# Kernel tuning notes

Hardware: AMD Instinct MI355X
Metric: run time of the kernel (lower is better)

## Reference

```python
import jax, jax.numpy as jnp
import numpy as np

B, L, D = 64, 128, 768          # batch, padded seq len, bert dim
H, HA = 1024, 256               # d_label_hidden, d_label_hidden_arc
POS, V = 18, 40                 # pos vocab, arc (deprel) vocab


def setup_inputs() -> dict:
    key = jax.random.key(0)
    ks = jax.random.split(key, 24)
    n = lambda i, shape, s=0.02: jax.random.normal(ks[i], shape, jnp.float32) * s
    # realistic padding: random sentence lengths in [L//2, L]
    lengths = jax.random.randint(ks[1], (B,), L // 2, L + 1)
    pad_mask = (jnp.arange(L)[None, :] < lengths[:, None]).astype(jnp.float32)
    heads = jax.random.randint(ks[2], (B, L), 0, L)
    # mark padded positions as -1 (zero head vector), as in the original loop
    heads = jnp.where(pad_mask > 0, heads, -1)
    return {
        "ann": jax.random.normal(ks[0], (B, L, D), jnp.float32),
        "pad_mask": pad_mask,
        "correct_heads": heads,
        # label-biaffine branch (hidden H)
        "W_head_mlp": n(3, (D, H)), "b_head_mlp": n(4, (H,)),
        "W_dep_mlp": n(5, (D, H)), "b_dep_mlp": n(6, (H,)),
        "W_lin": n(7, (H, H)), "b_lin": n(8, (H,)),
        "head_vec": n(9, (H,), 1.0), "dep_vec": n(10, (H,), 1.0),
        "bias": n(11, (1, 1, 1), 1.0),
        # arc-label biaffine branch (hidden HA, per-label bilinear)
        "W_head_arc_mlp": n(12, (D, HA)), "b_head_arc_mlp": n(13, (HA,)),
        "W_dep_arc_mlp": n(14, (D, HA)), "b_dep_arc_mlp": n(15, (HA,)),
        "W_arc": n(16, (V, HA, HA), 1.0),
        "head_vec_arc": n(17, (HA, V), 1.0), "dep_vec_arc": n(18, (HA, V), 1.0),
        "bias_arc": n(19, (1, 1, V), 1.0),
        # POS tip
        "W_pos": n(20, (D, POS)), "b_pos": n(21, (POS,)),
    }


def reference(ann, pad_mask, correct_heads,
              W_head_mlp, b_head_mlp, W_dep_mlp, b_dep_mlp,
              W_lin, b_lin, head_vec, dep_vec, bias,
              W_head_arc_mlp, b_head_arc_mlp, W_dep_arc_mlp, b_dep_arc_mlp,
              W_arc, head_vec_arc, dep_vec_arc, bias_arc,
              W_pos, b_pos):
    # POS prediction
    pos_pred = ann @ W_pos + b_pos                                  # [B,L,POS]

    # ---- dependency (unlabeled arc) biaffine ----
    ann_head = jax.nn.relu(ann @ W_head_mlp + b_head_mlp)           # [B,L,H]
    ann_dep = jax.nn.relu(ann @ W_dep_mlp + b_dep_mlp)              # [B,L,H]
    head_bias = ann_head @ head_vec                                 # [B,L]
    dep_bias = ann_dep @ dep_vec                                    # [B,L]
    Wh = ann_head @ W_lin + b_lin                                   # [B,L,H]
    # scores[b,i,j] = dep[b,i] . Wh[b,j]
    dep_W_headT = jnp.einsum('bih,bjh->bij', ann_dep, Wh)
    dep_W_headT = dep_W_headT + head_bias[:, None, :] + dep_bias[:, :, None] + bias
    valid_head = pad_mask[:, None, :] > 0                           # [B,1,L]
    dep_W_headT = jnp.where(valid_head, dep_W_headT, -jnp.inf)

    # ---- labeled arc biaffine (gather gold head per dependent) ----
    ann_head_arc = jax.nn.relu(ann @ W_head_arc_mlp + b_head_arc_mlp)  # [B,L,HA]
    ann_dep_arc = jax.nn.relu(ann @ W_dep_arc_mlp + b_dep_arc_mlp)     # [B,L,HA]
    idx = jnp.clip(correct_heads, 0, L - 1)
    gathered = jnp.take_along_axis(ann_head_arc, idx[:, :, None], axis=1)
    gathered = jnp.where((correct_heads == -1)[:, :, None], 0.0, gathered)  # [B,L,HA]

    head_arc_bias = gathered @ head_vec_arc                         # [B,L,V]
    dep_arc_bias = ann_dep_arc @ dep_vec_arc                        # [B,L,V]
    # per-label bilinear: s[b,l,v] = gathered[b,l] . W_arc[v] . dep[b,l]
    dep_W_headT_arc = jnp.einsum('bld,vde,ble->blv', gathered, W_arc, ann_dep_arc)
    dep_W_headT_arc = dep_W_headT_arc + head_arc_bias + dep_arc_bias + bias_arc

    return pos_pred, dep_W_headT, dep_W_headT_arc
```

## Files before the change

### kernel.cpp

```cpp
#include <hip/hip_runtime.h>
#include <hip/hip_bf16.h>

#define B_ 64
#define L_ 128
#define D_ 768
#define H_ 1024
#define HA_ 256
#define POS_ 18
#define V_ 40
#define BL_ (B_ * L_)

#define NEG_BIG (-1.0e30f)

typedef __attribute__((ext_vector_type(8))) short short8v;
typedef __attribute__((ext_vector_type(4))) short short4v;
typedef __attribute__((ext_vector_type(4))) float f32x4;

__device__ inline void split_bf16(float x, short& hi, short& lo) {
  __hip_bfloat16 h = __float2bfloat16(x);
  hi = *reinterpret_cast<short*>(&h);
  const float r = x - __bfloat162float(h);
  __hip_bfloat16 l = __float2bfloat16(r);
  lo = *reinterpret_cast<short*>(&l);
}

__device__ __forceinline__ short f2b(float x) {
  __hip_bfloat16 h = __float2bfloat16(x);
  return *reinterpret_cast<short*>(&h);
}
__device__ __forceinline__ float b2f(short s) {
  __hip_bfloat16 h = *reinterpret_cast<__hip_bfloat16*>(&s);
  return __bfloat162float(h);
}

__device__ __forceinline__ int swz8(int row, int s) { return ((s + (row >> 1)) & 3) * 8; }
__device__ __forceinline__ int colswz(int row, int n) {
  return (n & ~31) + swz8(row, (n >> 3) & 3) + (n & 7);
}

__device__ __forceinline__ void ld_lds16(const void* g, void* l) {
  __builtin_amdgcn_global_load_lds(
      (const __attribute__((address_space(1))) unsigned int*)g,
      (__attribute__((address_space(3))) unsigned int*)l, 16, 0, 0);
}

template<bool RELU, bool HASBIAS>
__global__ __launch_bounds__(256)
void gemm_bias(const float* __restrict__ A, const float* __restrict__ Bm,
               const float* __restrict__ bias, float* __restrict__ C,
               int M, int N, int K) {
  __shared__ __align__(16) float As[16][68];
  __shared__ __align__(16) float Bs[16][68];
  const int t = threadIdx.x;
  const int tx = t & 15, ty = t >> 4;
  const int m0 = blockIdx.y * 64, n0 = blockIdx.x * 64;
  const int arow = t >> 2, aks = (t & 3) * 4;
  const int bkr = t >> 4, bns = (t & 15) * 4;
  float acc[4][4] = {};
  for (int k0 = 0; k0 < K; k0 += 16) {
    const float4 av = *reinterpret_cast<const float4*>(&A[(size_t)(m0 + arow) * K + k0 + aks]);
    float4 bv;
    const int nb = n0 + bns;
    if (nb + 3 < N) {
      bv = *reinterpret_cast<const float4*>(&Bm[(size_t)(k0 + bkr) * N + nb]);
    } else {
      bv.x = (nb + 0 < N) ? Bm[(size_t)(k0 + bkr) * N + nb + 0] : 0.f;
      bv.y = (nb + 1 < N) ? Bm[(size_t)(k0 + bkr) * N + nb + 1] : 0.f;
      bv.z = (nb + 2 < N) ? Bm[(size_t)(k0 + bkr) * N + nb + 2] : 0.f;
      bv.w = 0.f;
    }
    __syncthreads();
    As[aks + 0][arow] = av.x;
    As[aks + 1][arow] = av.y;
    As[aks + 2][arow] = av.z;
    As[aks + 3][arow] = av.w;
    *reinterpret_cast<float4*>(&Bs[bkr][bns]) = bv;
    __syncthreads();
#pragma unroll
    for (int kk = 0; kk < 16; ++kk) {
      const float4 a4 = *reinterpret_cast<const float4*>(&As[kk][ty * 4]);
      const float4 b4 = *reinterpret_cast<const float4*>(&Bs[kk][tx * 4]);
      const float aa[4] = {a4.x, a4.y, a4.z, a4.w};
      const float bb[4] = {b4.x, b4.y, b4.z, b4.w};
#pragma unroll
      for (int i = 0; i < 4; ++i)
#pragma unroll
        for (int j = 0; j < 4; ++j)
          acc[i][j] = fmaf(aa[i], bb[j], acc[i][j]);
    }
  }
#pragma unroll
  for (int j = 0; j < 4; ++j) {
    const int n = n0 + tx * 4 + j;
    if (n >= N) continue;
    float bj = 0.f;
    if constexpr (HASBIAS) bj = bias[n];
#pragma unroll
    for (int i = 0; i < 4; ++i) {
      const int m = m0 + ty * 4 + i;
      float v = acc[i][j] + bj;
      if (RELU) v = fmaxf(v, 0.f);
      C[(size_t)m * N + n] = v;
    }
  }
}

__global__ __launch_bounds__(256)
void split_pre(const float* __restrict__ src, short* __restrict__ hi,
               short* __restrict__ lo, int K) {
  const int t = threadIdx.x;
  const int r = blockIdx.x * 4 + (t >> 6);
  const int lane = t & 63;
  for (int c = lane * 4; c < K; c += 256) {
    const float4 v = *reinterpret_cast<const float4*>(&src[(size_t)r * K + c]);
    const float vv[4] = {v.x, v.y, v.z, v.w};
    short4v h4, l4;
#pragma unroll
    for (int j = 0; j < 4; ++j) {
      short h, l;
      split_bf16(vv[j], h, l);
      h4[j] = h; l4[j] = l;
    }
    const int cs = colswz(r, c);
    *reinterpret_cast<short4v*>(&hi[(size_t)r * K + cs]) = h4;
    *reinterpret_cast<short4v*>(&lo[(size_t)r * K + cs]) = l4;
  }
}

__global__ __launch_bounds__(256)
void megaprep(const float* __restrict__ Whm, const float* __restrict__ Wdm,
              const float* __restrict__ Wlin, const float* __restrict__ Wha,
              const float* __restrict__ Wda, const float* __restrict__ Wpos,
              short* __restrict__ Thm, short* __restrict__ Tdm,
              short* __restrict__ Tlin, short* __restrict__ Tha,
              short* __restrict__ Tda, short* __restrict__ Pth,
              short* __restrict__ Ptl) {
  __shared__ float tile[32][33];
  const int bid = blockIdx.x;
  const int t = threadIdx.x;
  if (bid < 2944) {
    const float* W; short* T; int K, N, local;
    if (bid < 768)       { W = Whm;  T = Thm;  K = D_; N = H_;  local = bid; }
    else if (bid < 1536) { W = Wdm;  T = Tdm;  K = D_; N = H_;  local = bid - 768; }
    else if (bid < 2560) { W = Wlin; T = Tlin; K = H_; N = H_;  local = bid - 1536; }
    else if (bid < 2752) { W = Wha;  T = Tha;  K = D_; N = HA_; local = bid - 2560; }
    else                 { W = Wda;  T = Tda;  K = D_; N = HA_; local = bid - 2752; }
    const int ntiles = N >> 5;
    const int n0 = (local % ntiles) * 32;
    const int k0 = (local / ntiles) * 32;
    const int r = t >> 3, c = (t & 7) * 4;
    const float4 w4 = *reinterpret_cast<const float4*>(&W[(size_t)(k0 + r) * N + n0 + c]);
    tile[r][c + 0] = w4.x;
    tile[r][c + 1] = w4.y;
    tile[r][c + 2] = w4.z;
    tile[r][c + 3] = w4.w;
    __syncthreads();
    short4v hi4;
#pragma unroll
    for (int j = 0; j < 4; ++j) hi4[j] = f2b(tile[c + j][r]);
    const int row = n0 + r;
    const int cs = swz8(row, (c >> 3) & 3) + (c & 7);
    *reinterpret_cast<short4v*>(&T[(size_t)row * K + k0 + cs]) = hi4;
  } else {
    const int k0 = (bid - 2944) * 32;
    const int n = t & 31;
    const int ks = (t >> 5) * 4;
#pragma unroll
    for (int j = 0; j < 4; ++j) {
      const int k = k0 + ks + j;
      const float v = (n < POS_) ? Wpos[(size_t)k * POS_ + n] : 0.f;
      short h, l;
      split_bf16(v, h, l);
      Pth[(size_t)n * D_ + colswz(n, k)] = h;
      Ptl[(size_t)n * D_ + colswz(n, k)] = l;
    }
  }
}

__global__ __launch_bounds__(256)
void gemm_h2x(const short* __restrict__ Ath, const short* __restrict__ Atl,
              const short* __restrict__ B1h, const short* __restrict__ B2h,
              const float* __restrict__ bias1h, const float* __restrict__ bias2h,
              short* __restrict__ O1h, short* __restrict__ O2h,
              const short* __restrict__ B1a, const short* __restrict__ B2a,
              const float* __restrict__ bias1a, const float* __restrict__ bias2a,
              float* __restrict__ O1a, float* __restrict__ O2a,
              const short* __restrict__ Pth, const short* __restrict__ Ptl,
              const float* __restrict__ bpos, float* __restrict__ outp) {
  __shared__ __align__(16) short AhP[2][2048];
  __shared__ __align__(16) short B1P[2][4096];
  __shared__ __align__(16) short B2P[2][4096];
  const int bid = blockIdx.x;
  const int t = threadIdx.x;
  const int lane = t & 63, w = t >> 6;
  const int fr = lane & 15, kgi = lane >> 4;
  const int drow = lane >> 2, dslot = lane & 3;

  if (bid < 1280) {
    const bool big = bid < 1024;
    const int N = big ? H_ : HA_;
    const int ntx = N >> 7;
    const int local = big ? bid : bid - 1024;
    const int m0 = (local / ntx) * 64, n0 = (local % ntx) * 128;
    const short* B1t = big ? B1h : B1a;
    const short* B2t = big ? B2h : B2a;
    const float* bias1v = big ? bias1h : bias1a;
    const float* bias2v = big ? bias2h : bias2a;
    const int wm = w >> 1, wn = w & 1;
    f32x4 acc1[2][4] = {};
    f32x4 acc2[2][4] = {};

    auto stage = [&](int tt, int pb) {
      const int k0 = tt << 5;
      {
        const size_t ga = (size_t)(m0 + w * 16 + drow) * D_ + k0 + dslot * 8;
        ld_lds16(&Ath[ga], &AhP[pb][w * 512]);
      }
#pragma unroll
      for (int cc = 0; cc < 2; ++cc) {
        const int c = w * 2 + cc;
        const size_t gb = (size_t)(n0 + c * 16 + drow) * D_ + k0 + dslot * 8;
        ld_lds16(&B1t[gb], &B1P[pb][c * 512]);
        ld_lds16(&B2t[gb], &B2P[pb][c * 512]);
      }
    };
    auto compute = [&](int pb) {
      short8v ah[2];
#pragma unroll
      for (int mi = 0; mi < 2; ++mi) {
        const int r = wm * 32 + mi * 16 + fr;
        ah[mi] = *reinterpret_cast<const short8v*>(&AhP[pb][r * 32 + swz8(r, kgi)]);
      }
      __builtin_amdgcn_s_setprio(1);
#pragma unroll
      for (int nj = 0; nj < 4; ++nj) {
        const int rn = wn * 64 + nj * 16 + fr;
        const int sw = swz8(rn, kgi);
        const short8v b1 = *reinterpret_cast<const short8v*>(&B1P[pb][rn * 32 + sw]);
        const short8v b2 = *reinterpret_cast<const short8v*>(&B2P[pb][rn * 32 + sw]);
#pragma unroll
        for (int mi = 0; mi < 2; ++mi) {
          acc1[mi][nj] = __builtin_amdgcn_mfma_f32_16x16x32_bf16(ah[mi], b1, acc1[mi][nj], 0, 0, 0);
          acc2[mi][nj] = __builtin_amdgcn_mfma_f32_16x16x32_bf16(ah[mi], b2, acc2[mi][nj], 0, 0, 0);
        }
      }
      __builtin_amdgcn_s_setprio(0);
    };

    stage(0, 0);
    int cur = 0;
    for (int tt = 0; tt < 24; ++tt) {
      if (tt + 1 < 24) {
        stage(tt + 1, cur ^ 1);
        asm volatile("s_waitcnt vmcnt(5)" ::: "memory");
      } else {
        asm volatile("s_waitcnt vmcnt(0)" ::: "memory");
      }
      __builtin_amdgcn_s_barrier();
      compute(cur);
      __builtin_amdgcn_s_barrier();
      cur ^= 1;
    }

    const int rg = lane >> 4;
#pragma unroll
    for (int nj = 0; nj < 4; ++nj) {
      const int n = n0 + wn * 64 + nj * 16 + fr;
      const float b1 = bias1v[n];
      const float b2 = bias2v[n];
#pragma unroll
      for (int mi = 0; mi < 2; ++mi) {
#pragma unroll
        for (int q = 0; q < 4; ++q) {
          const int m = m0 + wm * 32 + mi * 16 + rg * 4 + q;
          const float v1 = fmaxf(acc1[mi][nj][q] + b1, 0.f);
          const float v2 = fmaxf(acc2[mi][nj][q] + b2, 0.f);
          if (big) {
            const size_t o = (size_t)m * N + colswz(m, n);
            O1h[o] = f2b(v1);
            O2h[o] = f2b(v2);
          } else {
            O1a[(size_t)m * N + n] = v1;
            O2a[(size_t)m * N + n] = v2;
          }
        }
      }
    }
  } else {
    const int m0 = (bid - 1280) * 64;
    f32x4 acc[2] = {};

    auto stage = [&](int tt, int pb) {
      const int k0 = tt << 5;
      const size_t ga = (size_t)(m0 + w * 16 + drow) * D_ + k0 + dslot * 8;
      ld_lds16(&Ath[ga], &AhP[pb][w * 512]);
      ld_lds16(&Atl[ga], &B1P[pb][w * 512]);
      {
        const short* bsrc = (w & 2) ? Ptl : Pth;
        const int c = w & 1;
        const size_t gb = (size_t)(c * 16 + drow) * D_ + k0 + dslot * 8;
        ld_lds16(&bsrc[gb], &B2P[pb][(w & 2) * 512 + c * 512]);
      }
    };
    auto compute = [&](int pb) {
      const int r = w * 16 + fr;
      const int swa = swz8(r, kgi);
      const short8v ah = *reinterpret_cast<const short8v*>(&AhP[pb][r * 32 + swa]);
      const short8v al = *reinterpret_cast<const short8v*>(&B1P[pb][r * 32 + swa]);
#pragma unroll
      for (int nj = 0; nj < 2; ++nj) {
        const int rn = nj * 16 + fr;
        const int sw = swz8(rn, kgi);
        const short8v bh = *reinterpret_cast<const short8v*>(&B2P[pb][rn * 32 + sw]);
        const short8v bl = *reinterpret_cast<const short8v*>(&B2P[pb][1024 + rn * 32 + sw]);
        acc[nj] = __builtin_amdgcn_mfma_f32_16x16x32_bf16(ah, bh, acc[nj], 0, 0, 0);
        acc[nj] = __builtin_amdgcn_mfma_f32_16x16x32_bf16(al, bh, acc[nj], 0, 0, 0);
        acc[nj] = __builtin_amdgcn_mfma_f32_16x16x32_bf16(ah, bl, acc[nj], 0, 0, 0);
      }
    };

    stage(0, 0);
    int cur = 0;
    for (int tt = 0; tt < 24; ++tt) {
      if (tt + 1 < 24) {
        stage(tt + 1, cur ^ 1);
        asm volatile("s_waitcnt vmcnt(3)" ::: "memory");
      } else {
        asm volatile("s_waitcnt vmcnt(0)" ::: "memory");
      }
      __builtin_amdgcn_s_barrier();
      compute(cur);
      __builtin_amdgcn_s_barrier();
      cur ^= 1;
    }

    const int rg = lane >> 4;
#pragma unroll
    for (int nj = 0; nj < 2; ++nj) {
      const int n = nj * 16 + fr;
      if (n >= POS_) continue;
      const float bj = bpos[n];
#pragma unroll
      for (int q = 0; q < 4; ++q) {
        const int m = m0 + w * 16 + rg * 4 + q;
        outp[(size_t)m * POS_ + n] = acc[nj][q] + bj;
      }
    }
  }
}

__global__ __launch_bounds__(256)
void lin_bias(const short* __restrict__ Ahh, const short* __restrict__ Bth,
              const float* __restrict__ bias, short* __restrict__ Oh,
              const short* __restrict__ Adh,
              const float* __restrict__ head_vec, const float* __restrict__ dep_vec,
              float* __restrict__ hb, float* __restrict__ db) {
  __shared__ __align__(16) short AhP[2][2048];
  __shared__ __align__(16) short BhP[2][4096];
  const int bid = blockIdx.x;
  const int t = threadIdx.x;
  const int lane = t & 63, w = t >> 6;

  if (bid < 1024) {
    const int m0 = (bid >> 3) * 64, n0 = (bid & 7) * 128;
    const int wm = w >> 1, wn = w & 1;
    const int fr = lane & 15, kgi = lane >> 4;
    const int drow = lane >> 2, dslot = lane & 3;
    f32x4 acc[2][4] = {};

    auto stage = [&](int tt, int pb) {
      const int k0 = tt << 5;
      {
        const size_t ga = (size_t)(m0 + w * 16 + drow) * H_ + k0 + dslot * 8;
        ld_lds16(&Ahh[ga], &AhP[pb][w * 512]);
      }
#pragma unroll
      for (int cc = 0; cc < 2; ++cc) {
        const int c = w * 2 + cc;
        const size_t gb = (size_t)(n0 + c * 16 + drow) * H_ + k0 + dslot * 8;
        ld_lds16(&Bth[gb], &BhP[pb][c * 512]);
      }
    };
    auto compute = [&](int pb) {
      short8v ah[2];
#pragma unroll
      for (int mi = 0; mi < 2; ++mi) {
        const int r = wm * 32 + mi * 16 + fr;
        ah[mi] = *reinterpret_cast<const short8v*>(&AhP[pb][r * 32 + swz8(r, kgi)]);
      }
      __builtin_amdgcn_s_setprio(1);
#pragma unroll
      for (int nj = 0; nj < 4; ++nj) {
        const int rn = wn * 64 + nj * 16 + fr;
        const short8v bh = *reinterpret_cast<const short8v*>(&BhP[pb][rn * 32 + swz8(rn, kgi)]);
#pragma unroll
        for (int mi = 0; mi < 2; ++mi)
          acc[mi][nj] = __builtin_amdgcn_mfma_f32_16x16x32_bf16(ah[mi], bh, acc[mi][nj], 0, 0, 0);
      }
      __builtin_amdgcn_s_setprio(0);
    };

    stage(0, 0);
    int cur = 0;
    for (int tt = 0; tt < 32; ++tt) {
      if (tt + 1 < 32) {
        stage(tt + 1, cur ^ 1);
        asm volatile("s_waitcnt vmcnt(3)" ::: "memory");
      } else {
        asm volatile("s_waitcnt vmcnt(0)" ::: "memory");
      }
      __builtin_amdgcn_s_barrier();
      compute(cur);
      __builtin_amdgcn_s_barrier();
      cur ^= 1;
    }

    const int rg = lane >> 4;
#pragma unroll
    for (int nj = 0; nj < 4; ++nj) {
      const int n = n0 + wn * 64 + nj * 16 + fr;
      const float bj = bias[n];
#pragma unroll
      for (int mi = 0; mi < 2; ++mi) {
#pragma unroll
        for (int q = 0; q < 4; ++q) {
          const int m = m0 + wm * 32 + mi * 16 + rg * 4 + q;
          Oh[(size_t)m * H_ + colswz(m, n)] = f2b(acc[mi][nj][q] + bj);
        }
      }
    }
  } else {
    const int m = (bid - 1024) * 4 + w;
    float sh = 0.f, sd = 0.f;
#pragma unroll
    for (int jj = 0; jj < 4; ++jj) {
      const int c = lane * 16 + jj * 4;
      const size_t o = (size_t)m * H_ + colswz(m, c);
      const short4v h4 = *reinterpret_cast<const short4v*>(&Ahh[o]);
      const short4v d4 = *reinterpret_cast<const short4v*>(&Adh[o]);
      const float4 hv = *reinterpret_cast<const float4*>(&head_vec[c]);
      const float4 dv = *reinterpret_cast<const float4*>(&dep_vec[c]);
      const float hvv[4] = {hv.x, hv.y, hv.z, hv.w};
      const float dvv[4] = {dv.x, dv.y, dv.z, dv.w};
#pragma unroll
      for (int j = 0; j < 4; ++j) {
        sh = fmaf(b2f(h4[j]), hvv[j], sh);
        sd = fmaf(b2f(d4[j]), dvv[j], sd);
      }
    }
#pragma unroll
    for (int off = 32; off; off >>= 1) {
      sh += __shfl_xor(sh, off);
      sd += __shfl_xor(sd, off);
    }
    if (lane == 0) {
      hb[m] = sh;
      db[m] = sd;
    }
  }
}

__global__ __launch_bounds__(256)
void scores_h(const short* __restrict__ Adh, const short* __restrict__ Whh,
              const float* __restrict__ hb, const float* __restrict__ db,
              const float* __restrict__ pad_mask, const float* __restrict__ bias1,
              float* __restrict__ out2) {
  __shared__ __align__(16) short AhP[2][2048];
  __shared__ __align__(16) short BhP[2][2048];
  const int t = threadIdx.x;
  const int b = blockIdx.z;
  const int i0 = blockIdx.y * 64, j0 = blockIdx.x * 64;
  const int lane = t & 63, w = t >> 6;
  const int wm = w >> 1, wn = w & 1;
  const int fr = lane & 15, kgi = lane >> 4;
  const int drow = lane >> 2, dslot = lane & 3;
  const size_t abase = ((size_t)b * L_ + i0) * H_;
  const size_t bbase = ((size_t)b * L_ + j0) * H_;
  f32x4 acc[2][2] = {};

  auto stage = [&](int tt, int pb) {
    const int k0 = tt << 5;
    const size_t ga = abase + (size_t)(w * 16 + drow) * H_ + k0 + dslot * 8;
    ld_lds16(&Adh[ga], &AhP[pb][w * 512]);
    const size_t gb = bbase + (size_t)(w * 16 + drow) * H_ + k0 + dslot * 8;
    ld_lds16(&Whh[gb], &BhP[pb][w * 512]);
  };
  auto compute = [&](int pb) {
    short8v ah[2];
#pragma unroll
    for (int mi = 0; mi < 2; ++mi) {
      const int r = wm * 32 + mi * 16 + fr;
      ah[mi] = *reinterpret_cast<const short8v*>(&AhP[pb][r * 32 + swz8(r, kgi)]);
    }
    __builtin_amdgcn_s_setprio(1);
#pragma unroll
    for (int nj = 0; nj < 2; ++nj) {
      const int rn = wn * 32 + nj * 16 + fr;
      const short8v bh = *reinterpret_cast<const short8v*>(&BhP[pb][rn * 32 + swz8(rn, kgi)]);
#pragma unroll
      for (int mi = 0; mi < 2; ++mi)
        acc[mi][nj] = __builtin_amdgcn_mfma_f32_16x16x32_bf16(ah[mi], bh, acc[mi][nj], 0, 0, 0);
    }
    __builtin_amdgcn_s_setprio(0);
  };

  stage(0, 0);
  int cur = 0;
  for (int tt = 0; tt < 32; ++tt) {
    if (tt + 1 < 32) {
      stage(tt + 1, cur ^ 1);
      asm volatile("s_waitcnt vmcnt(2)" ::: "memory");
    } else {
      asm volatile("s_waitcnt vmcnt(0)" ::: "memory");
    }
    __builtin_amdgcn_s_barrier();
    compute(cur);
    __builtin_amdgcn_s_barrier();
    cur ^= 1;
  }

  const int rg = lane >> 4;
  const float bias0 = bias1[0];
#pragma unroll
  for (int nj = 0; nj < 2; ++nj) {
    const int jcol = j0 + wn * 32 + nj * 16 + fr;
    const float mj = pad_mask[b * L_ + jcol];
    const float hbj = hb[b * L_ + jcol];
#pragma unroll
    for (int mi = 0; mi < 2; ++mi) {
#pragma unroll
      for (int q = 0; q < 4; ++q) {
        const int irow = i0 + wm * 32 + mi * 16 + rg * 4 + q;
        float v = acc[mi][nj][q] + hbj + db[b * L_ + irow] + bias0;
        if (!(mj > 0.f)) v = NEG_BIG;
        out2[((size_t)b * L_ + irow) * L_ + jcol] = v;
      }
    }
  }
}

__global__ __launch_bounds__(256)
void arcprep(const float* __restrict__ Warc, const float* __restrict__ dv,
             const float* __restrict__ head_arcb, const int* __restrict__ heads,
             short* __restrict__ WtA, float* __restrict__ dvT,
             float* __restrict__ g32, short* __restrict__ g_hi) {
  __shared__ float tile[32][33];
  const int bid = blockIdx.x;
  const int t = threadIdx.x;
  if (bid < 2560) {
    const int v = bid >> 6, rem = bid & 63;
    const int d0 = (rem >> 3) * 32, e0 = (rem & 7) * 32;
    const int r = t >> 3, c = (t & 7) * 4;
    const float4 w4 = *reinterpret_cast<const float4*>(
        &Warc[((size_t)v * HA_ + d0 + r) * HA_ + e0 + c]);
    tile[r][c + 0] = w4.x;
    tile[r][c + 1] = w4.y;
    tile[r][c + 2] = w4.z;
    tile[r][c + 3] = w4.w;
    __syncthreads();
    short4v hi4;
#pragma unroll
    for (int j = 0; j < 4; ++j) hi4[j] = f2b(tile[c + j][r]);
    const int row = e0 + r;
    const int cs = swz8(row, (c >> 3) & 3) + (c & 7);
    *reinterpret_cast<short4v*>(&WtA[((size_t)v * HA_ + row) * HA_ + d0 + cs]) = hi4;
  } else if (bid < 2600) {
    const int v = bid - 2560;
    dvT[(size_t)v * HA_ + t] = dv[(size_t)t * V_ + v];
  } else {
    const int m = (bid - 2600) * 4 + (t >> 6);
    const int lane = t & 63;
    const int h = heads[m];
    float4 g4 = make_float4(0.f, 0.f, 0.f, 0.f);
    if (h >= 0)
      g4 = *reinterpret_cast<const float4*>(
          &head_arcb[((size_t)((m >> 7) * L_ + h)) * HA_ + lane * 4]);
    *reinterpret_cast<float4*>(&g32[(size_t)m * HA_ + lane * 4]) = g4;
    short4v hi4;
    const float gv[4] = {g4.x, g4.y, g4.z, g4.w};
#pragma unroll
    for (int j = 0; j < 4; ++j) hi4[j] = f2b(gv[j]);
    *reinterpret_cast<short4v*>(&g_hi[(size_t)m * HA_ + colswz(m, lane * 4)]) = hi4;
  }
}

__global__ __launch_bounds__(512)
void arc_h(const short* __restrict__ g_hi, const short* __restrict__ Wt_hi,
           const float* __restrict__ dep32, const float* __restrict__ hb_arc,
           const float* __restrict__ dvT, float* __restrict__ out3) {
  __shared__ __align__(16) short AhP[2][8192];
  __shared__ __align__(16) short BhP[2][8192];
  __shared__ float parts[256][2];
  const int t = threadIdx.x;
  const int bid = blockIdx.x;
  const int xcd = bid & 7;
  const int j = bid >> 3;
  const int m0 = (j / 5) * 256;
  const int v = xcd * 5 + (j % 5);
  const int lane = t & 63, w = t >> 6;
  const int wm = w >> 1, we = w & 1;
  const int fr = lane & 15, kgi = lane >> 4;
  const int drow = lane >> 2, dslot = lane & 3;
  const size_t wbase = (size_t)v * HA_ * HA_;

  f32x4 acc[4][8] = {};

  auto stage = [&](int tt, int pb) {
    const int k0 = tt << 5;
#pragma unroll
    for (int cc = 0; cc < 2; ++cc) {
      const int c = w * 2 + cc;
      const size_t ga = (size_t)(m0 + c * 16 + drow) * HA_ + k0 + dslot * 8;
      ld_lds16(&g_hi[ga], &AhP[pb][c * 512]);
      const size_t gb = wbase + (size_t)(c * 16 + drow) * HA_ + k0 + dslot * 8;
      ld_lds16(&Wt_hi[gb], &BhP[pb][c * 512]);
    }
  };
  auto compute = [&](int pb) {
    short8v ah[4];
#pragma unroll
    for (int mi = 0; mi < 4; ++mi) {
      const int r = wm * 64 + mi * 16 + fr;
      ah[mi] = *reinterpret_cast<const short8v*>(&AhP[pb][r * 32 + swz8(r, kgi)]);
    }
    __builtin_amdgcn_s_setprio(1);
#pragma unroll
    for (int ej = 0; ej < 8; ++ej) {
      const int rb = we * 128 + ej * 16 + fr;
      const short8v bh = *reinterpret_cast<const short8v*>(&BhP[pb][rb * 32 + swz8(rb, kgi)]);
#pragma unroll
      for (int mi = 0; mi < 4; ++mi)
        acc[mi][ej] = __builtin_amdgcn_mfma_f32_16x16x32_bf16(ah[mi], bh, acc[mi][ej], 0, 0, 0);
    }
    __builtin_amdgcn_s_setprio(0);
  };

  stage(0, 0);
  int cur = 0;
#pragma unroll
  for (int tt = 0; tt < 8; ++tt) {
    if (tt < 7) {
      stage(tt + 1, cur ^ 1);
      asm volatile("s_waitcnt vmcnt(4)" ::: "memory");
    } else {
      asm volatile("s_waitcnt vmcnt(0)" ::: "memory");
    }
    __builtin_amdgcn_s_barrier();
    compute(cur);
    __builtin_amdgcn_s_barrier();
    cur ^= 1;
  }

  const int rg = lane >> 4;
  float dvr[8];
#pragma unroll
  for (int ej = 0; ej < 8; ++ej)
    dvr[ej] = dvT[(size_t)v * HA_ + we * 128 + ej * 16 + fr];
#pragma unroll
  for (int mi = 0; mi < 4; ++mi) {
#pragma unroll
    for (int q = 0; q < 4; ++q) {
      const int mrow = wm * 64 + mi * 16 + rg * 4 + q;
      const int m = m0 + mrow;
      float s = 0.f;
#pragma unroll
      for (int ej = 0; ej < 8; ++ej)
        s = fmaf(acc[mi][ej][q] + dvr[ej],
                 dep32[(size_t)m * HA_ + we * 128 + ej * 16 + fr], s);
      s += __shfl_xor(s, 1, 16);
      s += __shfl_xor(s, 2, 16);
      s += __shfl_xor(s, 4, 16);
      s += __shfl_xor(s, 8, 16);
      if (fr == 0) parts[mrow][we] = s;
    }
  }
  __syncthreads();
  if (t < 256) {
    const int m = m0 + t;
    out3[(size_t)m * V_ + v] = parts[t][0] + parts[t][1] + hb_arc[(size_t)m * V_ + v];
  }
}

extern "C" void kernel_launch(void* const* d_in, const int* in_sizes, int n_in,
                              void* d_out, int out_size, void* d_ws, size_t ws_size,
                              hipStream_t stream) {
  const float* ann        = (const float*)d_in[0];
  const float* pad_mask   = (const float*)d_in[1];
  const int*   heads      = (const int*)d_in[2];
  const float* W_head_mlp = (const float*)d_in[3];
  const float* b_head_mlp = (const float*)d_in[4];
  const float* W_dep_mlp  = (const float*)d_in[5];
  const float* b_dep_mlp  = (const float*)d_in[6];
  const float* W_lin      = (const float*)d_in[7];
  const float* b_lin      = (const float*)d_in[8];
  const float* head_vec   = (const float*)d_in[9];
  const float* dep_vec    = (const float*)d_in[10];
  const float* bias1      = (const float*)d_in[11];
  const float* W_head_arc = (const float*)d_in[12];
  const float* b_head_arc = (const float*)d_in[13];
  const float* W_dep_arc  = (const float*)d_in[14];
  const float* b_dep_arc  = (const float*)d_in[15];
  const float* W_arc      = (const float*)d_in[16];
  const float* hv_arc     = (const float*)d_in[17];
  const float* dv_arc     = (const float*)d_in[18];
  const float* bias_arc   = (const float*)d_in[19];
  const float* W_pos      = (const float*)d_in[20];
  const float* b_pos      = (const float*)d_in[21];

  float* out_pos    = (float*)d_out;
  float* out_scores = out_pos + (size_t)BL_ * POS_;
  float* out_arc    = out_scores + (size_t)B_ * L_ * L_;

  float* ws  = (float*)d_ws;
  float* R1  = ws;
  float* R2  = R1 + (size_t)BL_ * H_;
  float* R3  = R2 + (size_t)BL_ * H_;
  float* head_arcb = R3 + (size_t)BL_ * H_;
  float* dep_arcb  = head_arcb + (size_t)BL_ * HA_;
  float* hb        = dep_arcb + (size_t)BL_ * HA_;
  float* db        = hb + BL_;
  short* wt0     = (short*)(db + BL_);
  short* Wth_hm  = wt0;
  short* Wth_dm  = Wth_hm + (size_t)H_ * D_;
  short* Wth_lin = Wth_dm + (size_t)H_ * D_;
  short* Wth_ha  = Wth_lin + (size_t)H_ * H_;
  short* Wth_da  = Wth_ha + (size_t)HA_ * D_;
  short* Pth     = Wth_da + (size_t)HA_ * D_;
  short* Ptl     = Pth + (size_t)32 * D_;
  short* Ahh = (short*)R1;
  short* Adh = (short*)R2;
  short* Ath = (short*)R3;  short* Atl = Ath + (size_t)BL_ * D_;
  short* Whh = (short*)R3;
  float* g32 = (float*)wt0;
  short* Wt_hi  = (short*)R1;
  short* g_hi   = Wt_hi + (size_t)V_ * HA_ * HA_;
  float* hb_arc = (float*)(g_hi + (size_t)BL_ * HA_);
  float* dvT    = hb_arc + (size_t)BL_ * V_;

  const dim3 blk(256);
  split_pre<<<dim3(BL_ / 4), blk, 0, stream>>>(ann, Ath, Atl, D_);
  megaprep<<<dim3(2968), blk, 0, stream>>>(
      W_head_mlp, W_dep_mlp, W_lin, W_head_arc, W_dep_arc, W_pos,
      Wth_hm, Wth_dm, Wth_lin, Wth_ha, Wth_da, Pth, Ptl);

  gemm_h2x<<<dim3(1408), blk, 0, stream>>>(
      Ath, Atl, Wth_hm, Wth_dm, b_head_mlp, b_dep_mlp, Ahh, Adh,
      Wth_ha, Wth_da, b_head_arc, b_dep_arc, head_arcb, dep_arcb,
      Pth, Ptl, b_pos, out_pos);

  lin_bias<<<dim3(3072), blk, 0, stream>>>(
      Ahh, Wth_lin, b_lin, Whh, Adh, head_vec, dep_vec, hb, db);

  scores_h<<<dim3(2, 2, B_), blk, 0, stream>>>(
      Adh, Whh, hb, db, pad_mask, bias1, out_scores);

  arcprep<<<dim3(4648), blk, 0, stream>>>(
      W_arc, dv_arc, head_arcb, heads, Wt_hi, dvT, g32, g_hi);
  gemm_bias<false, true><<<dim3(1, BL_ / 64), blk, 0, stream>>>(
      g32, hv_arc, bias_arc, hb_arc, BL_, V_, HA_);
  arc_h<<<dim3((BL_ / 256) * V_), dim3(512), 0, stream>>>(
      g_hi, Wt_hi, dep_arcb, hb_arc, dvT, out_arc);
}
```

Baseline: 243.8 us.

## Merge arc-prep and scores kernels, compute head-arc bias before gather

The head-arc bias GEMM now runs on the ungathered head_arcb inside extra blocks of lin_bias, and arc_h gathers that bias through the gold head index. The gather fp32 copy g32 is no longer written. scores_h and arcprep are folded into a single scoresarc launch with block-index dispatch, which removes two launches and lets the small arc-prep work share the GPU with the scores GEMM. The cost is larger heterogeneous kernels and an extra indexed load in the arc_h epilogue.

```diff
diff --git a/kernel.cpp b/kernel.cpp
--- a/kernel.cpp
+++ b/kernel.cpp
@@ -42,67 +42,6 @@
   __builtin_amdgcn_global_load_lds(
       (const __attribute__((address_space(1))) unsigned int*)g,
       (__attribute__((address_space(3))) unsigned int*)l, 16, 0, 0);
-}
-
-template<bool RELU, bool HASBIAS>
-__global__ __launch_bounds__(256)
-void gemm_bias(const float* __restrict__ A, const float* __restrict__ Bm,
-               const float* __restrict__ bias, float* __restrict__ C,
-               int M, int N, int K) {
-  __shared__ __align__(16) float As[16][68];
-  __shared__ __align__(16) float Bs[16][68];
-  const int t = threadIdx.x;
-  const int tx = t & 15, ty = t >> 4;
-  const int m0 = blockIdx.y * 64, n0 = blockIdx.x * 64;
-  const int arow = t >> 2, aks = (t & 3) * 4;
-  const int bkr = t >> 4, bns = (t & 15) * 4;
-  float acc[4][4] = {};
-  for (int k0 = 0; k0 < K; k0 += 16) {
-    const float4 av = *reinterpret_cast<const float4*>(&A[(size_t)(m0 + arow) * K + k0 + aks]);
-    float4 bv;
-    const int nb = n0 + bns;
-    if (nb + 3 < N) {
-      bv = *reinterpret_cast<const float4*>(&Bm[(size_t)(k0 + bkr) * N + nb]);
-    } else {
-      bv.x = (nb + 0 < N) ? Bm[(size_t)(k0 + bkr) * N + nb + 0] : 0.f;
-      bv.y = (nb + 1 < N) ? Bm[(size_t)(k0 + bkr) * N + nb + 1] : 0.f;
-      bv.z = (nb + 2 < N) ? Bm[(size_t)(k0 + bkr) * N + nb + 2] : 0.f;
-      bv.w = 0.f;
-    }
-    __syncthreads();
-    As[aks + 0][arow] = av.x;
-    As[aks + 1][arow] = av.y;
-    As[aks + 2][arow] = av.z;
-    As[aks + 3][arow] = av.w;
-    *reinterpret_cast<float4*>(&Bs[bkr][bns]) = bv;
-    __syncthreads();
-#pragma unroll
-    for (int kk = 0; kk < 16; ++kk) {
-      const float4 a4 = *reinterpret_cast<const float4*>(&As[kk][ty * 4]);
-      const float4 b4 = *reinterpret_cast<const float4*>(&Bs[kk][tx * 4]);
-      const float aa[4] = {a4.x, a4.y, a4.z, a4.w};
-      const float bb[4] = {b4.x, b4.y, b4.z, b4.w};
-#pragma unroll
-      for (int i = 0; i < 4; ++i)
-#pragma unroll
-        for (int j = 0; j < 4; ++j)
-          acc[i][j] = fmaf(aa[i], bb[j], acc[i][j]);
-    }
-  }
-#pragma unroll
-  for (int j = 0; j < 4; ++j) {
-    const int n = n0 + tx * 4 + j;
-    if (n >= N) continue;
-    float bj = 0.f;
-    if constexpr (HASBIAS) bj = bias[n];
-#pragma unroll
-    for (int i = 0; i < 4; ++i) {
-      const int m = m0 + ty * 4 + i;
-      float v = acc[i][j] + bj;
-      if (RELU) v = fmaxf(v, 0.f);
-      C[(size_t)m * N + n] = v;
-    }
-  }
 }
 
 __global__ __launch_bounds__(256)
@@ -354,7 +293,9 @@
               const float* __restrict__ bias, short* __restrict__ Oh,
               const short* __restrict__ Adh,
               const float* __restrict__ head_vec, const float* __restrict__ dep_vec,
-              float* __restrict__ hb, float* __restrict__ db) {
+              float* __restrict__ hb, float* __restrict__ db,
+              const float* __restrict__ head_arcb, const float* __restrict__ hv_arc,
+              const float* __restrict__ bias_arc, float* __restrict__ hbase) {
   __shared__ __align__(16) short AhP[2][2048];
   __shared__ __align__(16) short BhP[2][4096];
   const int bid = blockIdx.x;
@@ -429,7 +370,7 @@
         }
       }
     }
-  } else {
+  } else if (bid < 3072) {
     const int m = (bid - 1024) * 4 + w;
     float sh = 0.f, sd = 0.f;
 #pragma unroll
@@ -457,98 +398,151 @@
       hb[m] = sh;
       db[m] = sd;
     }
+  } else {
+    float* Asf = (float*)AhP;
+    float* Bsf = (float*)BhP;
+    const int m0 = (bid - 3072) * 64;
+    const int tx = t & 15, ty = t >> 4;
+    const int arow = t >> 2, aks = (t & 3) * 4;
+    const int bkr = t >> 4, bns = (t & 15) * 4;
+    float acc[4][4] = {};
+    for (int k0 = 0; k0 < HA_; k0 += 16) {
+      const float4 av = *reinterpret_cast<const float4*>(
+          &head_arcb[(size_t)(m0 + arow) * HA_ + k0 + aks]);
+      float4 bv;
+      const int nb = bns;
+      if (nb + 3 < V_) {
+        bv = *reinterpret_cast<const float4*>(&hv_arc[(size_t)(k0 + bkr) * V_ + nb]);
+      } else {
+        bv.x = (nb + 0 < V_) ? hv_arc[(size_t)(k0 + bkr) * V_ + nb + 0] : 0.f;
+        bv.y = (nb + 1 < V_) ? hv_arc[(size_t)(k0 + bkr) * V_ + nb + 1] : 0.f;
+        bv.z = (nb + 2 < V_) ? hv_arc[(size_t)(k0 + bkr) * V_ + nb + 2] : 0.f;
+        bv.w = 0.f;
+      }
+      __syncthreads();
+      Asf[(aks + 0) * 68 + arow] = av.x;
+      Asf[(aks + 1) * 68 + arow] = av.y;
+      Asf[(aks + 2) * 68 + arow] = av.z;
+      Asf[(aks + 3) * 68 + arow] = av.w;
+      Bsf[bkr * 68 + bns + 0] = bv.x;
+      Bsf[bkr * 68 + bns + 1] = bv.y;
+      Bsf[bkr * 68 + bns + 2] = bv.z;
+      Bsf[bkr * 68 + bns + 3] = bv.w;
+      __syncthreads();
+#pragma unroll
+      for (int kk = 0; kk < 16; ++kk) {
+        const float4 a4 = *reinterpret_cast<const float4*>(&Asf[kk * 68 + ty * 4]);
+        const float4 b4 = *reinterpret_cast<const float4*>(&Bsf[kk * 68 + tx * 4]);
+        const float aa[4] = {a4.x, a4.y, a4.z, a4.w};
+        const float bb[4] = {b4.x, b4.y, b4.z, b4.w};
+#pragma unroll
+        for (int i = 0; i < 4; ++i)
+#pragma unroll
+          for (int j = 0; j < 4; ++j)
+            acc[i][j] = fmaf(aa[i], bb[j], acc[i][j]);
+      }
+    }
+#pragma unroll
+    for (int j = 0; j < 4; ++j) {
+      const int n = tx * 4 + j;
+      if (n >= V_) continue;
+      const float bj = bias_arc[n];
+#pragma unroll
+      for (int i = 0; i < 4; ++i) {
+        const int m = m0 + ty * 4 + i;
+        hbase[(size_t)m * V_ + n] = acc[i][j] + bj;
+      }
+    }
   }
 }
 
 __global__ __launch_bounds__(256)
-void scores_h(const short* __restrict__ Adh, const short* __restrict__ Whh,
-              const float* __restrict__ hb, const float* __restrict__ db,
-              const float* __restrict__ pad_mask, const float* __restrict__ bias1,
-              float* __restrict__ out2) {
+void scoresarc(const short* __restrict__ Adh, const short* __restrict__ Whh,
+               const float* __restrict__ hb, const float* __restrict__ db,
+               const float* __restrict__ pad_mask, const float* __restrict__ bias1,
+               float* __restrict__ out2,
+               const float* __restrict__ Warc, const float* __restrict__ dv,
+               const float* __restrict__ head_arcb, const int* __restrict__ heads,
+               short* __restrict__ WtA, float* __restrict__ dvT,
+               short* __restrict__ g_hi) {
   __shared__ __align__(16) short AhP[2][2048];
   __shared__ __align__(16) short BhP[2][2048];
-  const int t = threadIdx.x;
-  const int b = blockIdx.z;
-  const int i0 = blockIdx.y * 64, j0 = blockIdx.x * 64;
-  const int lane = t & 63, w = t >> 6;
-  const int wm = w >> 1, wn = w & 1;
-  const int fr = lane & 15, kgi = lane >> 4;
-  const int drow = lane >> 2, dslot = lane & 3;
-  const size_t abase = ((size_t)b * L_ + i0) * H_;
-  const size_t bbase = ((size_t)b * L_ + j0) * H_;
-  f32x4 acc[2][2] = {};
-
-  auto stage = [&](int tt, int pb) {
-    const int k0 = tt << 5;
-    const size_t ga = abase + (size_t)(w * 16 + drow) * H_ + k0 + dslot * 8;
-    ld_lds16(&Adh[ga], &AhP[pb][w * 512]);
-    const size_t gb = bbase + (size_t)(w * 16 + drow) * H_ + k0 + dslot * 8;
-    ld_lds16(&Whh[gb], &BhP[pb][w * 512]);
-  };
-  auto compute = [&](int pb) {
-    short8v ah[2];
-#pragma unroll
-    for (int mi = 0; mi < 2; ++mi) {
-      const int r = wm * 32 + mi * 16 + fr;
-      ah[mi] = *reinterpret_cast<const short8v*>(&AhP[pb][r * 32 + swz8(r, kgi)]);
-    }
-    __builtin_amdgcn_s_setprio(1);
-#pragma unroll
-    for (int nj = 0; nj < 2; ++nj) {
-      const int rn = wn * 32 + nj * 16 + fr;
-      const short8v bh = *reinterpret_cast<const short8v*>(&BhP[pb][rn * 32 + swz8(rn, kgi)]);
-#pragma unroll
-      for (int mi = 0; mi < 2; ++mi)
-        acc[mi][nj] = __builtin_amdgcn_mfma_f32_16x16x32_bf16(ah[mi], bh, acc[mi][nj], 0, 0, 0);
-    }
-    __builtin_amdgcn_s_setprio(0);
-  };
-
-  stage(0, 0);
-  int cur = 0;
-  for (int tt = 0; tt < 32; ++tt) {
-    if (tt + 1 < 32) {
-      stage(tt + 1, cur ^ 1);
-      asm volatile("s_waitcnt vmcnt(2)" ::: "memory");
-    } else {
-      asm volatile("s_waitcnt vmcnt(0)" ::: "memory");
-    }
-    __builtin_amdgcn_s_barrier();
-    compute(cur);
-    __builtin_amdgcn_s_barrier();
-    cur ^= 1;
-  }
-
-  const int rg = lane >> 4;
-  const float bias0 = bias1[0];
-#pragma unroll
-  for (int nj = 0; nj < 2; ++nj) {
-    const int jcol = j0 + wn * 32 + nj * 16 + fr;
-    const float mj = pad_mask[b * L_ + jcol];
-    const float hbj = hb[b * L_ + jcol];
-#pragma unroll
-    for (int mi = 0; mi < 2; ++mi) {
-#pragma unroll
-      for (int q = 0; q < 4; ++q) {
-        const int irow = i0 + wm * 32 + mi * 16 + rg * 4 + q;
-        float v = acc[mi][nj][q] + hbj + db[b * L_ + irow] + bias0;
-        if (!(mj > 0.f)) v = NEG_BIG;
-        out2[((size_t)b * L_ + irow) * L_ + jcol] = v;
-      }
-    }
-  }
-}
-
-__global__ __launch_bounds__(256)
-void arcprep(const float* __restrict__ Warc, const float* __restrict__ dv,
-             const float* __restrict__ head_arcb, const int* __restrict__ heads,
-             short* __restrict__ WtA, float* __restrict__ dvT,
-             float* __restrict__ g32, short* __restrict__ g_hi) {
-  __shared__ float tile[32][33];
   const int bid = blockIdx.x;
   const int t = threadIdx.x;
-  if (bid < 2560) {
-    const int v = bid >> 6, rem = bid & 63;
+  const int lane = t & 63, w = t >> 6;
+
+  if (bid < 256) {
+    const int j0 = (bid & 1) * 64, i0 = ((bid >> 1) & 1) * 64, b = bid >> 2;
+    const int wm = w >> 1, wn = w & 1;
+    const int fr = lane & 15, kgi = lane >> 4;
+    const int drow = lane >> 2, dslot = lane & 3;
+    const size_t abase = ((size_t)b * L_ + i0) * H_;
+    const size_t bbase = ((size_t)b * L_ + j0) * H_;
+    f32x4 acc[2][2] = {};
+
+    auto stage = [&](int tt, int pb) {
+      const int k0 = tt << 5;
+      const size_t ga = abase + (size_t)(w * 16 + drow) * H_ + k0 + dslot * 8;
+      ld_lds16(&Adh[ga], &AhP[pb][w * 512]);
+      const size_t gb = bbase + (size_t)(w * 16 + drow) * H_ + k0 + dslot * 8;
+      ld_lds16(&Whh[gb], &BhP[pb][w * 512]);
+    };
+    auto compute = [&](int pb) {
+      short8v ah[2];
+#pragma unroll
+      for (int mi = 0; mi < 2; ++mi) {
+        const int r = wm * 32 + mi * 16 + fr;
+        ah[mi] = *reinterpret_cast<const short8v*>(&AhP[pb][r * 32 + swz8(r, kgi)]);
+      }
+      __builtin_amdgcn_s_setprio(1);
+#pragma unroll
+      for (int nj = 0; nj < 2; ++nj) {
+        const int rn = wn * 32 + nj * 16 + fr;
+        const short8v bh = *reinterpret_cast<const short8v*>(&BhP[pb][rn * 32 + swz8(rn, kgi)]);
+#pragma unroll
+        for (int mi = 0; mi < 2; ++mi)
+          acc[mi][nj] = __builtin_amdgcn_mfma_f32_16x16x32_bf16(ah[mi], bh, acc[mi][nj], 0, 0, 0);
+      }
+      __builtin_amdgcn_s_setprio(0);
+    };
+
+    stage(0, 0);
+    int cur = 0;
+    for (int tt = 0; tt < 32; ++tt) {
+      if (tt + 1 < 32) {
+        stage(tt + 1, cur ^ 1);
+        asm volatile("s_waitcnt vmcnt(2)" ::: "memory");
+      } else {
+        asm volatile("s_waitcnt vmcnt(0)" ::: "memory");
+      }
+      __builtin_amdgcn_s_barrier();
+      compute(cur);
+      __builtin_amdgcn_s_barrier();
+      cur ^= 1;
+    }
+
+    const int rg = lane >> 4;
+    const float bias0 = bias1[0];
+#pragma unroll
+    for (int nj = 0; nj < 2; ++nj) {
+      const int jcol = j0 + wn * 32 + nj * 16 + fr;
+      const float mj = pad_mask[b * L_ + jcol];
+      const float hbj = hb[b * L_ + jcol];
+#pragma unroll
+      for (int mi = 0; mi < 2; ++mi) {
+#pragma unroll
+        for (int q = 0; q < 4; ++q) {
+          const int irow = i0 + wm * 32 + mi * 16 + rg * 4 + q;
+          float v = acc[mi][nj][q] + hbj + db[b * L_ + irow] + bias0;
+          if (!(mj > 0.f)) v = NEG_BIG;
+          out2[((size_t)b * L_ + irow) * L_ + jcol] = v;
+        }
+      }
+    }
+  } else if (bid < 2816) {
+    __shared__ float tile[32][33];
+    const int lb = bid - 256;
+    const int v = lb >> 6, rem = lb & 63;
     const int d0 = (rem >> 3) * 32, e0 = (rem & 7) * 32;
     const int r = t >> 3, c = (t & 7) * 4;
     const float4 w4 = *reinterpret_cast<const float4*>(
@@ -564,18 +558,16 @@
     const int row = e0 + r;
     const int cs = swz8(row, (c >> 3) & 3) + (c & 7);
     *reinterpret_cast<short4v*>(&WtA[((size_t)v * HA_ + row) * HA_ + d0 + cs]) = hi4;
-  } else if (bid < 2600) {
-    const int v = bid - 2560;
+  } else if (bid < 2856) {
+    const int v = bid - 2816;
     dvT[(size_t)v * HA_ + t] = dv[(size_t)t * V_ + v];
   } else {
-    const int m = (bid - 2600) * 4 + (t >> 6);
-    const int lane = t & 63;
+    const int m = (bid - 2856) * 4 + w;
     const int h = heads[m];
     float4 g4 = make_float4(0.f, 0.f, 0.f, 0.f);
     if (h >= 0)
       g4 = *reinterpret_cast<const float4*>(
           &head_arcb[((size_t)((m >> 7) * L_ + h)) * HA_ + lane * 4]);
-    *reinterpret_cast<float4*>(&g32[(size_t)m * HA_ + lane * 4]) = g4;
     short4v hi4;
     const float gv[4] = {g4.x, g4.y, g4.z, g4.w};
 #pragma unroll
@@ -586,7 +578,8 @@
 
 __global__ __launch_bounds__(512)
 void arc_h(const short* __restrict__ g_hi, const short* __restrict__ Wt_hi,
-           const float* __restrict__ dep32, const float* __restrict__ hb_arc,
+           const float* __restrict__ dep32, const float* __restrict__ hbase,
+           const int* __restrict__ heads, const float* __restrict__ bias_arc,
            const float* __restrict__ dvT, float* __restrict__ out3) {
   __shared__ __align__(16) short AhP[2][8192];
   __shared__ __align__(16) short BhP[2][8192];
@@ -677,7 +670,10 @@
   __syncthreads();
   if (t < 256) {
     const int m = m0 + t;
-    out3[(size_t)m * V_ + v] = parts[t][0] + parts[t][1] + hb_arc[(size_t)m * V_ + v];
+    const int h = heads[m];
+    const float hbv = (h >= 0)
+        ? hbase[((size_t)((m >> 7) * L_ + h)) * V_ + v] : bias_arc[v];
+    out3[(size_t)m * V_ + v] = parts[t][0] + parts[t][1] + hbv;
   }
 }
 
@@ -731,11 +727,10 @@
   short* Adh = (short*)R2;
   short* Ath = (short*)R3;  short* Atl = Ath + (size_t)BL_ * D_;
   short* Whh = (short*)R3;
-  float* g32 = (float*)wt0;
+  float* hbase = R2 + (size_t)BL_ * H_ / 2;
+  float* dvT   = hbase + (size_t)BL_ * V_;
   short* Wt_hi  = (short*)R1;
   short* g_hi   = Wt_hi + (size_t)V_ * HA_ * HA_;
-  float* hb_arc = (float*)(g_hi + (size_t)BL_ * HA_);
-  float* dvT    = hb_arc + (size_t)BL_ * V_;
 
   const dim3 blk(256);
   split_pre<<<dim3(BL_ / 4), blk, 0, stream>>>(ann, Ath, Atl, D_);
@@ -748,16 +743,14 @@
       Wth_ha, Wth_da, b_head_arc, b_dep_arc, head_arcb, dep_arcb,
       Pth, Ptl, b_pos, out_pos);
 
-  lin_bias<<<dim3(3072), blk, 0, stream>>>(
-      Ahh, Wth_lin, b_lin, Whh, Adh, head_vec, dep_vec, hb, db);
-
-  scores_h<<<dim3(2, 2, B_), blk, 0, stream>>>(
-      Adh, Whh, hb, db, pad_mask, bias1, out_scores);
-
-  arcprep<<<dim3(4648), blk, 0, stream>>>(
-      W_arc, dv_arc, head_arcb, heads, Wt_hi, dvT, g32, g_hi);
-  gemm_bias<false, true><<<dim3(1, BL_ / 64), blk, 0, stream>>>(
-      g32, hv_arc, bias_arc, hb_arc, BL_, V_, HA_);
+  lin_bias<<<dim3(3200), blk, 0, stream>>>(
+      Ahh, Wth_lin, b_lin, Whh, Adh, head_vec, dep_vec, hb, db,
+      head_arcb, hv_arc, bias_arc, hbase);
+
+  scoresarc<<<dim3(4904), blk, 0, stream>>>(
+      Adh, Whh, hb, db, pad_mask, bias1, out_scores,
+      W_arc, dv_arc, head_arcb, heads, Wt_hi, dvT, g_hi);
+
   arc_h<<<dim3((BL_ / 256) * V_), dim3(512), 0, stream>>>(
-      g_hi, Wt_hi, dep_arcb, hb_arc, dvT, out_arc);
-}
+      g_hi, Wt_hi, dep_arcb, hbase, heads, bias_arc, dvT, out_arc);
+}
```

After: 241.9 us. About the same (-0.7%).
